# Kernel tuning notes

Measured on AMD Instinct MI355X. Metric: run time of the kernel, lower is better.

Reference implementation:

```python
import jax, jax.numpy as jnp
import numpy as np

L, C = 256, 20
BATCH = 1024


def _pairwise_mask(L, C, mask_type='pairwise'):
    # mask[l1, c1, l2, c2] nonzero iff positions interact (l2 - l1 >= 1, or == 1 for neighbor)
    ls = jnp.arange(L)
    d = ls[None, :] - ls[:, None]  # [L, L] = l2 - l1
    m = (d >= 1) if mask_type == 'pairwise' else (d == 1)
    return jnp.broadcast_to(m[:, None, :, None], (L, C, L, C)).astype(jnp.float32)


def setup_inputs() -> dict:
    key = jax.random.key(0)
    k1, k2, k3 = jax.random.split(key, 3)
    x_lc = jax.random.uniform(k1, (BATCH, L * C), dtype=jnp.float32)
    theta_0 = jnp.zeros((1,), dtype=jnp.float32)
    theta_lc = jax.random.normal(k2, (L, C), dtype=jnp.float32) / np.sqrt(L)
    theta_lclc = jax.random.normal(k3, (L, C, L, C), dtype=jnp.float32) / np.sqrt(L * L)
    return {"x_lc": x_lc, "theta_0": theta_0, "theta_lc": theta_lc, "theta_lclc": theta_lclc}


def reference(x_lc, theta_0, theta_lc, theta_lclc):
    Ld, Cd = theta_lc.shape
    mask = _pairwise_mask(Ld, Cd, 'pairwise')
    # additive term: sum_lc theta_lc * x_lc  -> [B, 1]
    lin = x_lc @ theta_lc.reshape(Ld * Cd)  # [B]
    # pairwise term: x^T (theta * mask) x, expressed as a masked GEMM instead of a
    # broadcasted [B, L, C, L, C] product
    Theta = (theta_lclc * mask).reshape(Ld * Cd, Ld * Cd)  # [LC, LC]
    xm = x_lc @ Theta  # [B, LC]
    quad = jnp.sum(xm * x_lc, axis=1)  # [B]
    phi = theta_0 + (lin + quad)[:, None]  # [B, 1]
    return phi
```

## Files before the change

### kernel.cpp

```cpp
#include <hip/hip_runtime.h>
#include <hip/hip_bf16.h>
#include <cstdint>
#include <cstddef>

#define LCN 5120
#define BN  1024
#define CN  20

typedef __attribute__((ext_vector_type(4))) float  floatx4;
typedef __attribute__((ext_vector_type(8))) short  shortx8;
typedef __attribute__((ext_vector_type(4))) unsigned short ushortx4;

static __device__ __forceinline__ unsigned short f2bf(float f) {
    __hip_bfloat16 h = __float2bfloat16(f);
    return *reinterpret_cast<unsigned short*>(&h);
}

static __device__ __forceinline__ void gload_lds16(const void* g, void* l) {
    __builtin_amdgcn_global_load_lds(
        (const __attribute__((address_space(1))) void*)g,
        (__attribute__((address_space(3))) void*)l,
        16, 0, 0);
}

__global__ __launch_bounds__(256) void k_conv(const float* __restrict__ th,
                                              unsigned short* __restrict__ Tn) {
    const int a  = blockIdx.y;
    const int t  = a >> 7;
    const int c0 = (CN * ((128 * t) / CN + 1)) / 512;
    const int bx = blockIdx.x;
    if (2 * (bx + 1) <= c0) return;
    const int kmin = CN * (a / CN + 1);
    const int col  = bx * 1024 + threadIdx.x * 4;
    const floatx4 v = *reinterpret_cast<const floatx4*>(th + (size_t)a * LCN + col);
    ushortx4 o;
#pragma unroll
    for (int e = 0; e < 4; ++e)
        o[e] = (col + e >= kmin) ? f2bf(v[e]) : (unsigned short)0;
    *reinterpret_cast<ushortx4*>(Tn + (size_t)a * LCN + col) = o;
}

__global__ __launch_bounds__(256) void k_init(const float* __restrict__ x,
                                              const float* __restrict__ th0,
                                              const float* __restrict__ thlc,
                                              float* __restrict__ out,
                                              unsigned short* __restrict__ Xb) {
    const int b = blockIdx.x;
    const int tid = threadIdx.x;
    const floatx4* xr = reinterpret_cast<const floatx4*>(x + (size_t)b * LCN);
    const floatx4* tr = reinterpret_cast<const floatx4*>(thlc);
    ushortx4* xw = reinterpret_cast<ushortx4*>(Xb + (size_t)b * LCN);
    float s = 0.0f;
    for (int k = tid; k < LCN / 4; k += 256) {
        const floatx4 a = xr[k], t2 = tr[k];
        s += a[0] * t2[0] + a[1] * t2[1] + a[2] * t2[2] + a[3] * t2[3];
        ushortx4 o;
#pragma unroll
        for (int e = 0; e < 4; ++e) o[e] = f2bf(a[e]);
        xw[k] = o;
    }
#pragma unroll
    for (int off = 32; off > 0; off >>= 1) s += __shfl_down(s, off, 64);
    __shared__ float ws4[4];
    if ((tid & 63) == 0) ws4[tid >> 6] = s;
    __syncthreads();
    if (tid == 0) out[b] = th0[0] + ws4[0] + ws4[1] + ws4[2] + ws4[3];
}

__global__ __launch_bounds__(256) void k_quad(
    const unsigned short* __restrict__ Xb,
    const unsigned short* __restrict__ Tn,
    float*                __restrict__ out,
    const int tot)
{
    const int bid  = blockIdx.x;
    const int xcd  = bid & 7;
    const int slot = bid >> 3;
    const int m    = slot & 7;
    const int g    = slot >> 3;
    int q = g * 8 + xcd;
    if (q >= tot) return;

    __shared__ unsigned short As[128 * 32];
    __shared__ unsigned short Bs[128 * 32];
    __shared__ float partial[128];

    const int tid  = threadIdx.x;
    const int lane = tid & 63;
    const int w    = tid >> 6;
    const int wm   = w & 1;
    const int wn   = w >> 1;
    const int lrow = lane & 15;
    const int kq   = lane >> 4;

    int n = 0, c = 0;
    for (int t = 0; t < 40; ++t) {
        const int c0t = (CN * ((128 * t) / CN + 1)) / 512;
        const int chn = 10 - c0t;
        if (q < chn) { n = t; c = c0t + q; break; }
        q -= chn;
    }
    const int b0 = m * 128;
    const int n0 = n * 128;
    const int k0 = c * 512;

    if (tid < 128) partial[tid] = 0.0f;

    floatx4 acc[4][4];
#pragma unroll
    for (int mt = 0; mt < 4; ++mt)
#pragma unroll
        for (int nt = 0; nt < 4; ++nt) acc[mt][nt] = (floatx4)0.0f;

    int aoff[4], boff[4];
#pragma unroll
    for (int mt = 0; mt < 4; ++mt) {
        const int row = wm * 64 + mt * 16 + lrow;
        aoff[mt] = row * 32 + (((kq + (row >> 1)) & 3) << 3);
    }
#pragma unroll
    for (int nt = 0; nt < 4; ++nt) {
        const int row = wn * 64 + nt * 16 + lrow;
        boff[nt] = row * 32 + (((kq + (row >> 1)) & 3) << 3);
    }

    for (int kk = 0; kk < 16; ++kk) {
        const int kc = k0 + kk * 32;
#pragma unroll
        for (int t = 0; t < 2; ++t) {
            const int s    = t * 256 + tid;
            const int row  = s >> 2;
            const int gseg = ((s & 3) - (row >> 1)) & 3;
            char* la = (char*)As + (size_t)(t * 256 + w * 64) * 16;
            char* lb = (char*)Bs + (size_t)(t * 256 + w * 64) * 16;
            gload_lds16(Xb + (size_t)(b0 + row) * LCN + kc + gseg * 8, la);
            gload_lds16(Tn + (size_t)(n0 + row) * LCN + kc + gseg * 8, lb);
        }
        __syncthreads();

        shortx8 af[4], bfr[4];
#pragma unroll
        for (int mt = 0; mt < 4; ++mt)
            af[mt] = *reinterpret_cast<const shortx8*>(As + aoff[mt]);
#pragma unroll
        for (int nt = 0; nt < 4; ++nt)
            bfr[nt] = *reinterpret_cast<const shortx8*>(Bs + boff[nt]);
#pragma unroll
        for (int mt = 0; mt < 4; ++mt)
#pragma unroll
            for (int nt = 0; nt < 4; ++nt)
                acc[mt][nt] = __builtin_amdgcn_mfma_f32_16x16x32_bf16(af[mt], bfr[nt], acc[mt][nt], 0, 0, 0);
        __syncthreads();
    }

#pragma unroll
    for (int mt = 0; mt < 4; ++mt) {
#pragma unroll
        for (int r = 0; r < 4; ++r) {
            const int b = b0 + wm * 64 + mt * 16 + kq * 4 + r;
            float s = 0.0f;
#pragma unroll
            for (int nt = 0; nt < 4; ++nt) {
                const int a = n0 + wn * 64 + nt * 16 + lrow;
                const __hip_bfloat16 hv = *reinterpret_cast<const __hip_bfloat16*>(&Xb[(size_t)b * LCN + a]);
                s += acc[mt][nt][r] * __bfloat162float(hv);
            }
            s += __shfl_xor(s, 1, 64);
            s += __shfl_xor(s, 2, 64);
            s += __shfl_xor(s, 4, 64);
            s += __shfl_xor(s, 8, 64);
            if (lrow == 0) atomicAdd(&partial[b - b0], s);
        }
    }
    __syncthreads();
    if (tid < 128) atomicAdd(&out[b0 + tid], partial[tid]);
}

extern "C" void kernel_launch(void* const* d_in, const int* in_sizes, int n_in,
                              void* d_out, int out_size, void* d_ws, size_t ws_size,
                              hipStream_t stream) {
    const float* x      = (const float*)d_in[0];
    const float* th0    = (const float*)d_in[1];
    const float* thlc   = (const float*)d_in[2];
    const float* thlclc = (const float*)d_in[3];
    float* out = (float*)d_out;

    unsigned short* Tn = (unsigned short*)d_ws;
    unsigned short* Xb = (unsigned short*)((char*)d_ws + (size_t)LCN * LCN * 2);

    k_conv<<<dim3(LCN / 1024, LCN), 256, 0, stream>>>(thlclc, Tn);
    k_init<<<dim3(BN), 256, 0, stream>>>(x, th0, thlc, out, Xb);

    int tot = 0;
    for (int t = 0; t < 40; ++t) {
        const int c0t = (CN * ((128 * t) / CN + 1)) / 512;
        tot += 10 - c0t;
    }
    const int groups = (tot + 7) / 8;
    k_quad<<<dim3(groups * 64), 256, 0, stream>>>(Xb, Tn, out, tot);
}
```

Before: 233.5 us.

## Double-buffer LDS tiles in k_quad to overlap global loads with MFMA

Splits the A and B shared-memory tiles into two buffers. The loads for step k+1 are issued straight into the alternate buffer while the MFMAs for step k run, replacing the load-sync-compute-sync loop with a single barrier per iteration. Per-thread load offsets are precomputed once. This doubles LDS use per block, which may lower occupancy, and overlap is limited because each barrier still waits for all outstanding loads.

Measured after the change: 232.1 us. No clear change (-0.6%).

```diff
diff --git a/kernel.cpp b/kernel.cpp
--- a/kernel.cpp
+++ b/kernel.cpp
@@ -81,8 +81,8 @@
     int q = g * 8 + xcd;
     if (q >= tot) return;
 
-    __shared__ unsigned short As[128 * 32];
-    __shared__ unsigned short Bs[128 * 32];
+    __shared__ unsigned short As[2][128 * 32];
+    __shared__ unsigned short Bs[2][128 * 32];
     __shared__ float partial[128];
 
     const int tid  = threadIdx.x;
@@ -112,6 +112,16 @@
 #pragma unroll
         for (int nt = 0; nt < 4; ++nt) acc[mt][nt] = (floatx4)0.0f;
 
+    int grow[2], goff[2], loff[2];
+#pragma unroll
+    for (int t = 0; t < 2; ++t) {
+        const int s    = t * 256 + tid;
+        const int row  = s >> 2;
+        const int gseg = ((s & 3) - (row >> 1)) & 3;
+        grow[t] = row;
+        goff[t] = gseg * 8;
+        loff[t] = (t * 256 + w * 64) * 16;
+    }
     int aoff[4], boff[4];
 #pragma unroll
     for (int mt = 0; mt < 4; ++mt) {
@@ -124,33 +134,35 @@
         boff[nt] = row * 32 + (((kq + (row >> 1)) & 3) << 3);
     }
 
+#pragma unroll
+    for (int t = 0; t < 2; ++t) {
+        gload_lds16(Xb + (size_t)(b0 + grow[t]) * LCN + k0 + goff[t], (char*)As[0] + loff[t]);
+        gload_lds16(Tn + (size_t)(n0 + grow[t]) * LCN + k0 + goff[t], (char*)Bs[0] + loff[t]);
+    }
+
     for (int kk = 0; kk < 16; ++kk) {
-        const int kc = k0 + kk * 32;
-#pragma unroll
-        for (int t = 0; t < 2; ++t) {
-            const int s    = t * 256 + tid;
-            const int row  = s >> 2;
-            const int gseg = ((s & 3) - (row >> 1)) & 3;
-            char* la = (char*)As + (size_t)(t * 256 + w * 64) * 16;
-            char* lb = (char*)Bs + (size_t)(t * 256 + w * 64) * 16;
-            gload_lds16(Xb + (size_t)(b0 + row) * LCN + kc + gseg * 8, la);
-            gload_lds16(Tn + (size_t)(n0 + row) * LCN + kc + gseg * 8, lb);
+        const int p = kk & 1;
+        __syncthreads();
+        if (kk < 15) {
+            const int kc = k0 + (kk + 1) * 32;
+#pragma unroll
+            for (int t = 0; t < 2; ++t) {
+                gload_lds16(Xb + (size_t)(b0 + grow[t]) * LCN + kc + goff[t], (char*)As[p ^ 1] + loff[t]);
+                gload_lds16(Tn + (size_t)(n0 + grow[t]) * LCN + kc + goff[t], (char*)Bs[p ^ 1] + loff[t]);
+            }
         }
-        __syncthreads();
-
         shortx8 af[4], bfr[4];
 #pragma unroll
         for (int mt = 0; mt < 4; ++mt)
-            af[mt] = *reinterpret_cast<const shortx8*>(As + aoff[mt]);
+            af[mt] = *reinterpret_cast<const shortx8*>(As[p] + aoff[mt]);
 #pragma unroll
         for (int nt = 0; nt < 4; ++nt)
-            bfr[nt] = *reinterpret_cast<const shortx8*>(Bs + boff[nt]);
+            bfr[nt] = *reinterpret_cast<const shortx8*>(Bs[p] + boff[nt]);
 #pragma unroll
         for (int mt = 0; mt < 4; ++mt)
 #pragma unroll
             for (int nt = 0; nt < 4; ++nt)
                 acc[mt][nt] = __builtin_amdgcn_mfma_f32_16x16x32_bf16(af[mt], bfr[nt], acc[mt][nt], 0, 0, 0);
-        __syncthreads();
     }
 
 #pragma unroll
```

## Load MFMA operands directly from global memory, dropping LDS staging and barriers

Applied to the files above, without the earlier changes.

Removes the LDS tiles and the per-iteration global_load_lds staging with its two barriers. Each lane now reads its bf16 A and B fragments straight from global memory, and the 16-step K loop is fully unrolled so the compiler can issue loads early. This removes synchronisation and LDS traffic, but each tile element is now fetched by both waves that share it, which raises global/L2 traffic. It also uses more registers because loads are in flight across the unrolled loop.

New measurement: 281.4 us. 20.5% more time.

```diff
diff --git a/kernel.cpp b/kernel.cpp
--- a/kernel.cpp
+++ b/kernel.cpp
@@ -14,13 +14,6 @@
 static __device__ __forceinline__ unsigned short f2bf(float f) {
     __hip_bfloat16 h = __float2bfloat16(f);
     return *reinterpret_cast<unsigned short*>(&h);
-}
-
-static __device__ __forceinline__ void gload_lds16(const void* g, void* l) {
-    __builtin_amdgcn_global_load_lds(
-        (const __attribute__((address_space(1))) void*)g,
-        (__attribute__((address_space(3))) void*)l,
-        16, 0, 0);
 }
 
 __global__ __launch_bounds__(256) void k_conv(const float* __restrict__ th,
@@ -81,8 +74,6 @@
     int q = g * 8 + xcd;
     if (q >= tot) return;
 
-    __shared__ unsigned short As[128 * 32];
-    __shared__ unsigned short Bs[128 * 32];
     __shared__ float partial[128];
 
     const int tid  = threadIdx.x;
@@ -112,46 +103,32 @@
 #pragma unroll
         for (int nt = 0; nt < 4; ++nt) acc[mt][nt] = (floatx4)0.0f;
 
-    int aoff[4], boff[4];
+    const unsigned short* ap[4];
+    const unsigned short* bp[4];
 #pragma unroll
-    for (int mt = 0; mt < 4; ++mt) {
-        const int row = wm * 64 + mt * 16 + lrow;
-        aoff[mt] = row * 32 + (((kq + (row >> 1)) & 3) << 3);
-    }
+    for (int mt = 0; mt < 4; ++mt)
+        ap[mt] = Xb + (size_t)(b0 + wm * 64 + mt * 16 + lrow) * LCN + k0 + kq * 8;
 #pragma unroll
-    for (int nt = 0; nt < 4; ++nt) {
-        const int row = wn * 64 + nt * 16 + lrow;
-        boff[nt] = row * 32 + (((kq + (row >> 1)) & 3) << 3);
-    }
+    for (int nt = 0; nt < 4; ++nt)
+        bp[nt] = Tn + (size_t)(n0 + wn * 64 + nt * 16 + lrow) * LCN + k0 + kq * 8;
 
+#pragma unroll
     for (int kk = 0; kk < 16; ++kk) {
-        const int kc = k0 + kk * 32;
-#pragma unroll
-        for (int t = 0; t < 2; ++t) {
-            const int s    = t * 256 + tid;
-            const int row  = s >> 2;
-            const int gseg = ((s & 3) - (row >> 1)) & 3;
-            char* la = (char*)As + (size_t)(t * 256 + w * 64) * 16;
-            char* lb = (char*)Bs + (size_t)(t * 256 + w * 64) * 16;
-            gload_lds16(Xb + (size_t)(b0 + row) * LCN + kc + gseg * 8, la);
-            gload_lds16(Tn + (size_t)(n0 + row) * LCN + kc + gseg * 8, lb);
-        }
-        __syncthreads();
-
         shortx8 af[4], bfr[4];
 #pragma unroll
         for (int mt = 0; mt < 4; ++mt)
-            af[mt] = *reinterpret_cast<const shortx8*>(As + aoff[mt]);
+            af[mt] = *reinterpret_cast<const shortx8*>(ap[mt] + kk * 32);
 #pragma unroll
         for (int nt = 0; nt < 4; ++nt)
-            bfr[nt] = *reinterpret_cast<const shortx8*>(Bs + boff[nt]);
+            bfr[nt] = *reinterpret_cast<const shortx8*>(bp[nt] + kk * 32);
 #pragma unroll
         for (int mt = 0; mt < 4; ++mt)
 #pragma unroll
             for (int nt = 0; nt < 4; ++nt)
                 acc[mt][nt] = __builtin_amdgcn_mfma_f32_16x16x32_bf16(af[mt], bfr[nt], acc[mt][nt], 0, 0, 0);
-        __syncthreads();
     }
+
+    __syncthreads();
 
 #pragma unroll
     for (int mt = 0; mt < 4; ++mt) {
```
